# Kernel optimization log

Hardware: AMD Instinct MI355X
Metric: run time of the kernel (lower is better)

## Reference

```python
import jax, jax.numpy as jnp
import numpy as np

D_MODEL = 1024
IDX_DIM = 64
SEQ = 4096
D_STATE = 64
EXPAND = 1
HEADDIM = 32
D_CONV = 4
D_INNER = EXPAND * D_MODEL
NHEADS = D_INNER // HEADDIM
CONV_DIM = D_INNER + 2 * D_STATE
D_IN_PROJ = 2 * D_INNER + 2 * D_STATE + NHEADS  # z, xBC, dt


def setup_inputs() -> dict:
    key = jax.random.key(0)
    ks = jax.random.split(key, 8)
    def rn(k, shape, scale=1.0):
        return jax.random.normal(k, shape, jnp.float32) * scale
    return {
        "x": rn(ks[0], (SEQ, D_MODEL)),
        "W_in": rn(ks[1], (D_IN_PROJ, D_MODEL), D_MODEL ** -0.5),
        "conv_w": rn(ks[2], (CONV_DIM, D_CONV), D_CONV ** -0.5),
        "conv_b": jnp.zeros((CONV_DIM,), jnp.float32),
        "dt_bias": rn(ks[3], (NHEADS,)),
        "A_log": jnp.log(jnp.arange(1, NHEADS + 1, dtype=jnp.float32)),
        "D": jnp.ones((NHEADS,), jnp.float32),
        "norm_w": jnp.ones((D_INNER,), jnp.float32),
        "W_out": rn(ks[4], (D_MODEL, D_INNER), D_INNER ** -0.5),
        "W_q": rn(ks[5], (IDX_DIM, D_MODEL), D_MODEL ** -0.5),
        "W_k": rn(ks[6], (IDX_DIM, D_MODEL), D_MODEL ** -0.5),
    }


def _silu(v):
    return v * jax.nn.sigmoid(v)


def _mamba2(x, W_in, conv_w, conv_b, dt_bias, A_log, Dp, norm_w, W_out):
    L = x.shape[0]
    zxbcdt = x @ W_in.T  # [L, D_IN_PROJ]
    z, xBC, dt = jnp.split(zxbcdt, [D_INNER, D_INNER + CONV_DIM], axis=-1)
    # depthwise causal conv1d, kernel D_CONV
    xc = jax.lax.conv_general_dilated(
        xBC.T[None],               # [1, C, L]
        conv_w[:, None, :],        # [C, 1, K]
        (1,), [(D_CONV - 1, 0)], feature_group_count=CONV_DIM)[0].T
    xBC = _silu(xc + conv_b)
    xs, B, C = jnp.split(xBC, [D_INNER, D_INNER + D_STATE], axis=-1)
    xs = xs.reshape(L, NHEADS, HEADDIM)
    dt = jax.nn.softplus(dt + dt_bias)   # [L, H]
    A = -jnp.exp(A_log)                  # [H]

    def step(h, inp):
        x_t, B_t, C_t, dt_t = inp        # [H,P], [N], [N], [H]
        dA = jnp.exp(dt_t * A)           # [H]
        h = h * dA[:, None, None] + (dt_t[:, None] * x_t)[:, :, None] * B_t[None, None, :]
        return h, jnp.einsum('hpn,n->hp', h, C_t)

    h0 = jnp.zeros((NHEADS, HEADDIM, D_STATE), x.dtype)
    _, ys = jax.lax.scan(step, h0, (xs, B, C, dt))  # ys: [L, H, P]
    y = ys + Dp[None, :, None] * xs
    y = y.reshape(L, D_INNER)
    y = y * _silu(z)                                 # gated RMSNorm
    y = y * jax.lax.rsqrt(jnp.mean(y * y, axis=-1, keepdims=True) + 1e-5) * norm_w
    return y @ W_out.T


def reference(x, W_in, conv_w, conv_b, dt_bias, A_log, D, norm_w, W_out, W_q, W_k):
    L = x.shape[0]
    x_mamba = _mamba2(x, W_in, conv_w, conv_b, dt_bias, A_log, D, norm_w, W_out)
    q = x_mamba @ W_q.T                  # [L, IDX_DIM]
    k = x @ W_k.T                        # [L, IDX_DIM]
    scores = jnp.einsum('ti,si->ts', q, k) * (IDX_DIM ** -0.5)
    mask = jnp.tril(jnp.ones((L, L), dtype=bool))
    return jnp.where(mask, scores, -jnp.inf)
```

## Files before the change

kernel.cpp:

```cpp
#include <hip/hip_runtime.h>
#include <math.h>

#define L_SEQ 4096
#define DMODEL 1024
#define DINNER 1024
#define DSTATE 64
#define NH 32
#define HD 32
#define CONVD 1152
#define DPROJ2 2272
#define KOFF 2208
#define QC 128
#define NC 32

#define NEG_FILL (-1e30f)

typedef __attribute__((ext_vector_type(8))) short short8;
typedef __attribute__((ext_vector_type(4))) float f32x4;
typedef unsigned short u16;

__device__ __forceinline__ u16 f2bf(float f) {
  unsigned int u = __float_as_uint(f);
  unsigned int r = (u + 0x7fffu + ((u >> 16) & 1u)) >> 16;
  return (u16)r;
}
__device__ __forceinline__ float bf2f(u16 b) {
  unsigned int u = ((unsigned int)b) << 16;
  return __uint_as_float(u);
}
__device__ __forceinline__ short8 pack8(float4 a, float4 b) {
  short8 v;
  v[0] = (short)f2bf(a.x); v[1] = (short)f2bf(a.y);
  v[2] = (short)f2bf(a.z); v[3] = (short)f2bf(a.w);
  v[4] = (short)f2bf(b.x); v[5] = (short)f2bf(b.y);
  v[6] = (short)f2bf(b.z); v[7] = (short)f2bf(b.w);
  return v;
}

__device__ __forceinline__ void g2l16(const void* g, void* l) {
  __builtin_amdgcn_global_load_lds(
      (const __attribute__((address_space(1))) unsigned int*)g,
      (__attribute__((address_space(3))) unsigned int*)l, 16, 0, 0);
}

#define CAST_N0 (L_SEQ * DMODEL / 8)
#define CAST_N1 (2208 * DMODEL / 8)
#define CAST_N2 (64 * DMODEL / 8)
#define CAST_TOTAL (CAST_N0 + CAST_N1 + 2 * CAST_N2)
#define CAST_BLKS (CAST_TOTAL / 256)
__global__ __launch_bounds__(256) void cast_tr_k(const float* __restrict__ x,
                                                 const float* __restrict__ W_in,
                                                 const float* __restrict__ W_k,
                                                 const float* __restrict__ W_q,
                                                 const float* __restrict__ W_out,
                                                 u16* __restrict__ x_bf,
                                                 u16* __restrict__ Wcat,
                                                 u16* __restrict__ Wq_bf,
                                                 u16* __restrict__ WoutT) {
  __shared__ float tile[64][65];
  int bid = blockIdx.x;
  if (bid < CAST_BLKS) {
    int gid = bid * 256 + threadIdx.x;
    const float* src;
    u16* dst;
    int i;
    if (gid < CAST_N0) { src = x; dst = x_bf; i = gid; }
    else if (gid < CAST_N0 + CAST_N1) { src = W_in; dst = Wcat; i = gid - CAST_N0; }
    else if (gid < CAST_N0 + CAST_N1 + CAST_N2) {
      src = W_k; dst = Wcat + (size_t)2208 * DMODEL; i = gid - CAST_N0 - CAST_N1;
    } else { src = W_q; dst = Wq_bf; i = gid - CAST_N0 - CAST_N1 - CAST_N2; }
    i *= 8;
    float4 f0 = *(const float4*)(src + i);
    float4 f1 = *(const float4*)(src + i + 4);
    *(short8*)(dst + i) = pack8(f0, f1);
    return;
  }
  bid -= CAST_BLKS;
  int bx = bid & 15, by = bid >> 4;
  int tx = threadIdx.x & 63, ty = threadIdx.x >> 6;
#pragma unroll
  for (int k = 0; k < 16; k++) {
    int r = ty + k * 4;
    tile[r][tx] = W_out[(size_t)(by * 64 + r) * 1024 + bx * 64 + tx];
  }
  __syncthreads();
#pragma unroll
  for (int k = 0; k < 16; k++) {
    int r = ty + k * 4;
    WoutT[(size_t)(bx * 64 + r) * 1024 + by * 64 + tx] = f2bf(tile[tx][r]);
  }
}

__global__ __launch_bounds__(256) void wqo_k(const u16* __restrict__ Wq,
                                             const u16* __restrict__ WoutT,
                                             const float* __restrict__ nw,
                                             u16* __restrict__ Wqo) {
  const int tid = threadIdx.x;
  const int wave = tid >> 6, lane = tid & 63;
  const int l15 = lane & 15, quad = lane >> 4;
  const int j0 = blockIdx.x * 64;
  f32x4 acc[4] = {};
  for (int kk = 0; kk < 32; kk++) {
    short8 b = *(const short8*)(WoutT + (size_t)(j0 + wave * 16 + l15) * 1024 + kk * 32 + quad * 8);
#pragma unroll
    for (int mi = 0; mi < 4; mi++) {
      short8 a = *(const short8*)(Wq + (size_t)(mi * 16 + l15) * 1024 + kk * 32 + quad * 8);
      acc[mi] = __builtin_amdgcn_mfma_f32_16x16x32_bf16(a, b, acc[mi], 0, 0, 0);
    }
  }
  int col = j0 + wave * 16 + l15;
  float w = nw[col];
#pragma unroll
  for (int mi = 0; mi < 4; mi++)
#pragma unroll
    for (int r = 0; r < 4; r++) {
      int i = mi * 16 + quad * 4 + r;
      Wqo[(size_t)i * 1024 + col] = f2bf(acc[mi][r] * w);
    }
}

__global__ __launch_bounds__(256) void gemm128(const u16* __restrict__ A,
                                               const u16* __restrict__ B,
                                               u16* __restrict__ Cbf,
                                               int M, int N, int K) {
  __shared__ u16 As[128 * 64];
  __shared__ u16 Bs[128 * 64];
  const int tid = threadIdx.x;
  const int wave = tid >> 6, lane = tid & 63;
  const int m0 = blockIdx.x * 128, n0 = blockIdx.y * 128;
  const int wm = (wave >> 1) * 64, wn = (wave & 1) * 64;
  const int l15 = lane & 15, quad = lane >> 4;

  const u16* aptr[4];
  const u16* bptr[4];
  char *ldsA[4], *ldsB[4];
#pragma unroll
  for (int b = 0; b < 4; b++) {
    int ch = b * 256 + tid;
    int row = ch >> 3, q = (ch & 7) ^ (row & 7);
    aptr[b] = A + (size_t)(m0 + row) * K + q * 8;
    int bn = min(n0 + row, N - 1);
    bptr[b] = B + (size_t)bn * K + q * 8;
    ldsA[b] = (char*)As + b * 4096 + wave * 1024;
    ldsB[b] = (char*)Bs + b * 4096 + wave * 1024;
  }

  int offA[2][4], offB[2][4];
#pragma unroll
  for (int kk = 0; kk < 2; kk++)
#pragma unroll
    for (int i = 0; i < 4; i++) {
      int ra = wm + i * 16 + l15;
      offA[kk][i] = ra * 64 + ((kk * 4 + quad) ^ (ra & 7)) * 8;
      int rb = wn + i * 16 + l15;
      offB[kk][i] = rb * 64 + ((kk * 4 + quad) ^ (rb & 7)) * 8;
    }

  f32x4 acc[4][4] = {};
  for (int k0 = 0; k0 < K; k0 += 64) {
#pragma unroll
    for (int b = 0; b < 4; b++) g2l16(aptr[b] + k0, ldsA[b]);
#pragma unroll
    for (int b = 0; b < 4; b++) g2l16(bptr[b] + k0, ldsB[b]);
    __builtin_amdgcn_s_waitcnt(0);
    __syncthreads();
#pragma unroll
    for (int kk = 0; kk < 2; kk++) {
      short8 af[4], bfr[4];
#pragma unroll
      for (int i = 0; i < 4; i++) af[i] = *(const short8*)(As + offA[kk][i]);
#pragma unroll
      for (int j = 0; j < 4; j++) bfr[j] = *(const short8*)(Bs + offB[kk][j]);
#pragma unroll
      for (int mi = 0; mi < 4; mi++)
#pragma unroll
        for (int ni = 0; ni < 4; ni++)
          acc[mi][ni] = __builtin_amdgcn_mfma_f32_16x16x32_bf16(af[mi], bfr[ni],
                                                                acc[mi][ni], 0, 0, 0);
    }
    __syncthreads();
  }
#pragma unroll
  for (int mi = 0; mi < 4; mi++)
#pragma unroll
    for (int r = 0; r < 4; r++) {
      int grow = m0 + wm + mi * 16 + quad * 4 + r;
#pragma unroll
      for (int ni = 0; ni < 4; ni++) {
        int gcol = n0 + wn + ni * 16 + l15;
        if (gcol < N) Cbf[(size_t)grow * N + gcol] = f2bf(acc[mi][ni][r]);
      }
    }
}

__global__ __launch_bounds__(256) void splitk64(const u16* __restrict__ A,
                                                const u16* __restrict__ B,
                                                float* __restrict__ P,
                                                int M, int K) {
  __shared__ u16 As[128 * 32];
  __shared__ u16 Bs[64 * 32];
  const int tid = threadIdx.x;
  const int wave = tid >> 6, lane = tid & 63;
  const int m0 = blockIdx.x * 128;
  const int ks = blockIdx.y;
  const int wm = (wave >> 1) * 64, wn = (wave & 1) * 32;
  const int l15 = lane & 15, quad = lane >> 4;

  const int c0 = tid, c1 = 256 + tid;
  const int r0 = c0 >> 2, q0 = (c0 & 3) ^ ((r0 >> 1) & 3);
  const int r1 = c1 >> 2, q1 = (c1 & 3) ^ ((r1 >> 1) & 3);
  const int rb = tid >> 2, qb = (tid & 3) ^ ((rb >> 1) & 3);
  const u16* a0 = A + (size_t)(m0 + r0) * K + q0 * 8;
  const u16* a1 = A + (size_t)(m0 + r1) * K + q1 * 8;
  const u16* bptr = B + (size_t)rb * K + qb * 8;
  char* ldsA0 = (char*)As + wave * 1024;
  char* ldsA1 = (char*)As + 4096 + wave * 1024;
  char* ldsB = (char*)Bs + wave * 1024;

  int offA[4], offB[2];
#pragma unroll
  for (int i = 0; i < 4; i++) {
    int ra = wm + i * 16 + l15;
    offA[i] = ra * 32 + (quad ^ ((ra >> 1) & 3)) * 8;
  }
#pragma unroll
  for (int j = 0; j < 2; j++) {
    int rr = wn + j * 16 + l15;
    offB[j] = rr * 32 + (quad ^ ((rr >> 1) & 3)) * 8;
  }

  f32x4 acc[4][2] = {};
  const int kbeg = ks * 128;
  for (int k0 = kbeg; k0 < kbeg + 128; k0 += 32) {
    g2l16(a0 + k0, ldsA0);
    g2l16(a1 + k0, ldsA1);
    g2l16(bptr + k0, ldsB);
    __builtin_amdgcn_s_waitcnt(0);
    __syncthreads();
    short8 af[4], bfr[2];
#pragma unroll
    for (int i = 0; i < 4; i++) af[i] = *(const short8*)(As + offA[i]);
#pragma unroll
    for (int j = 0; j < 2; j++) bfr[j] = *(const short8*)(Bs + offB[j]);
#pragma unroll
    for (int mi = 0; mi < 4; mi++)
#pragma unroll
      for (int ni = 0; ni < 2; ni++)
        acc[mi][ni] = __builtin_amdgcn_mfma_f32_16x16x32_bf16(af[mi], bfr[ni],
                                                              acc[mi][ni], 0, 0, 0);
    __syncthreads();
  }
  float* Pp = P + (size_t)ks * M * 64;
#pragma unroll
  for (int mi = 0; mi < 4; mi++)
#pragma unroll
    for (int r = 0; r < 4; r++) {
      int grow = m0 + wm + mi * 16 + quad * 4 + r;
#pragma unroll
      for (int ni = 0; ni < 2; ni++)
        Pp[(size_t)grow * 64 + wn + ni * 16 + l15] = acc[mi][ni][r];
    }
}

__global__ __launch_bounds__(256) void reduce8_k(const float* __restrict__ P,
                                                 const float* __restrict__ ssq,
                                                 u16* __restrict__ out, int n) {
  int i = blockIdx.x * 256 + threadIdx.x;
  if (i >= n) return;
  float s = 0.f;
#pragma unroll
  for (int ks = 0; ks < 8; ks++) s += P[(size_t)ks * n + i];
  float sc = rsqrtf(ssq[i >> 6] * (1.f / 1024.f) + 1e-5f);
  out[i] = f2bf(s * sc);
}

#define CONV_BLKS (L_SEQ * 144 / 256)
__global__ __launch_bounds__(256) void conv_dt_k(const u16* __restrict__ zx,
                                                 const float* __restrict__ cw,
                                                 const float* __restrict__ cb,
                                                 u16* __restrict__ xbc,
                                                 const float* __restrict__ dt_bias,
                                                 const float* __restrict__ A_log,
                                                 float* __restrict__ dtsp,
                                                 float* __restrict__ aL,
                                                 float* __restrict__ ssq) {
  if (blockIdx.x < CONV_BLKS) {
    int gid = blockIdx.x * 256 + threadIdx.x;
    int t = gid / 144;
    int c0 = (gid - t * 144) * 8;
    float acc[8];
#pragma unroll
    for (int j = 0; j < 8; j++) acc[j] = cb[c0 + j];
    float wv[8][4];
#pragma unroll
    for (int j = 0; j < 8; j++) {
      float4 w4 = *(const float4*)(cw + (c0 + j) * 4);
      wv[j][0] = w4.x; wv[j][1] = w4.y; wv[j][2] = w4.z; wv[j][3] = w4.w;
    }
#pragma unroll
    for (int k = 0; k < 4; k++) {
      int s = t - 3 + k;
      if (s >= 0) {
        short8 v = *(const short8*)(zx + (size_t)s * DPROJ2 + DINNER + c0);
#pragma unroll
        for (int j = 0; j < 8; j++) acc[j] += bf2f((u16)v[j]) * wv[j][k];
      }
    }
    short8 o;
#pragma unroll
    for (int j = 0; j < 8; j++) o[j] = (short)f2bf(acc[j] / (1.f + expf(-acc[j])));
    *(short8*)(xbc + (size_t)t * CONVD + c0) = o;
    return;
  }
  if (threadIdx.x < 16) ssq[(blockIdx.x - CONV_BLKS) * 16 + threadIdx.x] = 0.f;
  int w = threadIdx.x >> 6, lane = threadIdx.x & 63;
  int idx = (blockIdx.x - CONV_BLKS) * 4 + w;
  int h = idx & 31, c = idx >> 5;
  float negA = -expf(A_log[h]);
  float bias = dt_bias[h];
  float carry = 0.f;
#pragma unroll
  for (int seg = 0; seg < 2; seg++) {
    int t = c * QC + seg * 64 + lane;
    float xv = bf2f(zx[(size_t)t * DPROJ2 + 2176 + h]) + bias;
    float sp = (xv > 20.f) ? xv : log1pf(expf(xv));
    dtsp[(size_t)t * 32 + h] = sp;
    float v = sp * negA;
#pragma unroll
    for (int off = 1; off < 64; off <<= 1) {
      float u = __shfl_up(v, off, 64);
      if (lane >= off) v += u;
    }
    aL[(size_t)t * 32 + h] = carry + v;
    carry += __shfl(v, 63, 64);
  }
}

__global__ __launch_bounds__(256) void csg_k(const u16* __restrict__ xbc,
                                             const float* __restrict__ dtsp,
                                             const float* __restrict__ aL,
                                             float* __restrict__ S,
                                             float* __restrict__ G) {
  int tid = threadIdx.x;
  const int wave = tid >> 6, lane = tid & 63;
  const int l15 = lane & 15, quad = lane >> 4;
  __shared__ __align__(16) u16 sXs[32 * 136];
  __shared__ __align__(16) u16 sBT[64 * 136];
  __shared__ float scoef[QC];
  if (blockIdx.x < (unsigned)(NC * NH)) {
    int h = blockIdx.x & 31, c = blockIdx.x >> 5;
    if (tid < QC) {
      float aend = aL[(size_t)(c * QC + QC - 1) * 32 + h];
      float a = aL[(size_t)(c * QC + tid) * 32 + h];
      scoef[tid] = expf(aend - a) * dtsp[(size_t)(c * QC + tid) * 32 + h];
    }
    __syncthreads();
    for (int j = tid; j < 32 * QC / 8; j += 256) {
      int s = j & 127, p0 = (j >> 7) * 8;
      short8 v = *(const short8*)(xbc + (size_t)(c * QC + s) * CONVD + h * HD + p0);
      float cf = scoef[s];
#pragma unroll
      for (int e = 0; e < 8; e++) sXs[(p0 + e) * 136 + s] = f2bf(cf * bf2f((u16)v[e]));
    }
    for (int j = tid; j < 64 * QC / 8; j += 256) {
      int s = j & 127, n0 = (j >> 7) * 8;
      short8 v = *(const short8*)(xbc + (size_t)(c * QC + s) * CONVD + DINNER + n0);
#pragma unroll
      for (int e = 0; e < 8; e++) sBT[(n0 + e) * 136 + s] = (u16)v[e];
    }
    __syncthreads();
    f32x4 acc[2] = {};
#pragma unroll
    for (int kk = 0; kk < 4; kk++) {
      short8 b = *(const short8*)(sBT + (wave * 16 + l15) * 136 + kk * 32 + quad * 8);
#pragma unroll
      for (int i = 0; i < 2; i++) {
        short8 a = *(const short8*)(sXs + (i * 16 + l15) * 136 + kk * 32 + quad * 8);
        acc[i] = __builtin_amdgcn_mfma_f32_16x16x32_bf16(a, b, acc[i], 0, 0, 0);
      }
    }
    float* Sb = S + ((size_t)c * 32 + h) * 2048;
#pragma unroll
    for (int i = 0; i < 2; i++)
#pragma unroll
      for (int r = 0; r < 4; r++) {
        int p = i * 16 + quad * 4 + r;
        Sb[p * 64 + wave * 16 + l15] = acc[i][r];
      }
    return;
  }
  int c = blockIdx.x - NC * NH;
  const int wm = (wave >> 1) * 64, wn = (wave & 1) * 64;
  f32x4 acc[4][4] = {};
#pragma unroll
  for (int kk = 0; kk < 2; kk++) {
    short8 a[4], b[4];
#pragma unroll
    for (int i = 0; i < 4; i++) {
      int t = wm + i * 16 + l15;
      a[i] = *(const short8*)(xbc + (size_t)(c * QC + t) * CONVD + DINNER + DSTATE + kk * 32 + quad * 8);
      int s = wn + i * 16 + l15;
      b[i] = *(const short8*)(xbc + (size_t)(c * QC + s) * CONVD + DINNER + kk * 32 + quad * 8);
    }
#pragma unroll
    for (int mi = 0; mi < 4; mi++)
#pragma unroll
      for (int ni = 0; ni < 4; ni++)
        acc[mi][ni] = __builtin_amdgcn_mfma_f32_16x16x32_bf16(a[mi], b[ni],
                                                              acc[mi][ni], 0, 0, 0);
  }
  float* Gb = G + (size_t)c * QC * QC;
#pragma unroll
  for (int mi = 0; mi < 4; mi++)
#pragma unroll
    for (int r = 0; r < 4; r++) {
      int t = wm + mi * 16 + quad * 4 + r;
#pragma unroll
      for (int ni = 0; ni < 4; ni++)
        Gb[(size_t)t * QC + wn + ni * 16 + l15] = acc[mi][ni][r];
    }
}

__global__ __launch_bounds__(256) void state_scan_k(const float* __restrict__ S,
                                                    const float* __restrict__ aL,
                                                    float* __restrict__ Hinit) {
  int idx = blockIdx.x * 256 + threadIdx.x;
  int h = idx >> 11, rem = idx & 2047;
  float E = 0.f;
#pragma unroll
  for (int c = 0; c < NC; c++) {
    size_t o = ((size_t)c * 32 + h) * 2048 + rem;
    Hinit[o] = E;
    float dec = expf(aL[(size_t)(c * QC + QC - 1) * 32 + h]);
    E = E * dec + S[o];
  }
}

__global__ __launch_bounds__(256) void yout_mfma(const u16* __restrict__ xbc,
                                                 const float* __restrict__ dtsp,
                                                 const float* __restrict__ aL,
                                                 const float* __restrict__ G,
                                                 const float* __restrict__ Hinit,
                                                 const float* __restrict__ Dv,
                                                 const u16* __restrict__ zx,
                                                 float* __restrict__ ssq,
                                                 u16* __restrict__ y) {
  int h = blockIdx.x & 31, c = blockIdx.x >> 5;
  int tid = threadIdx.x;
  __shared__ __align__(16) u16 sXT[32 * 136];
  __shared__ float sa[QC];
  __shared__ float sd[QC];

  if (tid < QC) {
    sa[tid] = aL[(size_t)(c * QC + tid) * 32 + h];
    sd[tid] = dtsp[(size_t)(c * QC + tid) * 32 + h];
  }
  for (int j = tid; j < 32 * QC / 8; j += 256) {
    int t = j & 127, p0 = (j >> 7) * 8;
    short8 v = *(const short8*)(xbc + (size_t)(c * QC + t) * CONVD + h * HD + p0);
#pragma unroll
    for (int e = 0; e < 8; e++) sXT[(p0 + e) * 136 + t] = (u16)v[e];
  }
  __syncthreads();

  const int wave = tid >> 6, lane = tid & 63;
  const int l15 = lane & 15, quad = lane >> 4;
  f32x4 acc1[2][2] = {};
  f32x4 acc2[2][2] = {};

#pragma unroll
  for (int kk = 0; kk < 4; kk++) {
    short8 b[2];
#pragma unroll
    for (int j = 0; j < 2; j++)
      b[j] = *(const short8*)(sXT + (j * 16 + l15) * 136 + kk * 32 + quad * 8);
#pragma unroll
    for (int i = 0; i < 2; i++) {
      int rmax = wave * 32 + i * 16 + 15;
      if (kk * 32 > rmax) continue;
      int m = wave * 32 + i * 16 + l15;
      float am = sa[m];
      const float* Gp = G + (size_t)c * QC * QC + (size_t)m * QC + kk * 32 + quad * 8;
      float4 g0 = *(const float4*)Gp;
      float4 g1 = *(const float4*)(Gp + 4);
      float gv[8] = {g0.x, g0.y, g0.z, g0.w, g1.x, g1.y, g1.z, g1.w};
      int s0 = kk * 32 + quad * 8;
      short8 a;
#pragma unroll
      for (int j2 = 0; j2 < 8; j2++) {
        int s = s0 + j2;
        float w = 0.f;
        if (s <= m) w = expf(am - sa[s]) * sd[s] * gv[j2];
        a[j2] = (short)f2bf(w);
      }
#pragma unroll
      for (int j = 0; j < 2; j++)
        acc1[i][j] = __builtin_amdgcn_mfma_f32_16x16x32_bf16(a, b[j], acc1[i][j], 0, 0, 0);
    }
  }

  const float* Hbase = Hinit + ((size_t)c * 32 + h) * 2048;
#pragma unroll
  for (int kk = 0; kk < 2; kk++) {
    short8 b[2];
#pragma unroll
    for (int j = 0; j < 2; j++) {
      const float* Hp = Hbase + (size_t)(j * 16 + l15) * 64 + kk * 32 + quad * 8;
      b[j] = pack8(*(const float4*)Hp, *(const float4*)(Hp + 4));
    }
#pragma unroll
    for (int i = 0; i < 2; i++) {
      int t = wave * 32 + i * 16 + l15;
      short8 a = *(const short8*)(xbc + (size_t)(c * QC + t) * CONVD + DINNER + DSTATE + kk * 32 + quad * 8);
#pragma unroll
      for (int j = 0; j < 2; j++)
        acc2[i][j] = __builtin_amdgcn_mfma_f32_16x16x32_bf16(a, b[j], acc2[i][j], 0, 0, 0);
    }
  }

  float Dh = Dv[h];
#pragma unroll
  for (int i = 0; i < 2; i++) {
#pragma unroll
    for (int r = 0; r < 4; r++) {
      int t = wave * 32 + i * 16 + quad * 4 + r;
      float et = expf(sa[t]);
      float part = 0.f;
#pragma unroll
      for (int j = 0; j < 2; j++) {
        int p = j * 16 + l15;
        float xv = bf2f(sXT[p * 136 + t]);
        float val = acc1[i][j][r] + et * acc2[i][j][r] + Dh * xv;
        float z = bf2f(zx[(size_t)(c * QC + t) * DPROJ2 + h * HD + p]);
        float vg = val * (z / (1.f + expf(-z)));
        part += vg * vg;
        y[(size_t)(c * QC + t) * DINNER + h * HD + p] = f2bf(vg);
      }
      part += __shfl_xor(part, 1, 64);
      part += __shfl_xor(part, 2, 64);
      part += __shfl_xor(part, 4, 64);
      part += __shfl_xor(part, 8, 64);
      if (l15 == 0) atomicAdd(ssq + c * QC + t, part);
    }
  }
}

__global__ __launch_bounds__(256) void scores_mfma(const u16* __restrict__ q,
                                                   const u16* __restrict__ kmat,
                                                   int kstride,
                                                   float* __restrict__ out) {
  const int m0 = blockIdx.y * 128, n0 = blockIdx.x * 128;
  const int tid = threadIdx.x;
  if (n0 > m0 + 127) {
    f32x4 f = {NEG_FILL, NEG_FILL, NEG_FILL, NEG_FILL};
    for (int i = tid; i < 128 * 32; i += 256) {
      int row = i >> 5, c4 = (i & 31) << 2;
      __builtin_nontemporal_store(f, (f32x4*)(out + (size_t)(m0 + row) * L_SEQ + n0 + c4));
    }
    return;
  }
  const int wave = tid >> 6, lane = tid & 63;
  const int wm = (wave >> 1) * 64, wn = (wave & 1) * 64;
  const int l15 = lane & 15, quad = lane >> 4;
  f32x4 acc[4][4] = {};
#pragma unroll
  for (int kk = 0; kk < 2; kk++) {
    short8 a[4], b[4];
#pragma unroll
    for (int i = 0; i < 4; i++) {
      a[i] = *(const short8*)(q + (size_t)(m0 + wm + i * 16 + l15) * 64 + kk * 32 + quad * 8);
      b[i] = *(const short8*)(kmat + (size_t)(n0 + wn + i * 16 + l15) * kstride + kk * 32 + quad * 8);
    }
#pragma unroll
    for (int mi = 0; mi < 4; mi++)
#pragma unroll
      for (int ni = 0; ni < 4; ni++)
        acc[mi][ni] = __builtin_amdgcn_mfma_f32_16x16x32_bf16(a[mi], b[ni],
                                                              acc[mi][ni], 0, 0, 0);
  }
#pragma unroll
  for (int mi = 0; mi < 4; mi++)
#pragma unroll
    for (int r = 0; r < 4; r++) {
      int row = m0 + wm + mi * 16 + quad * 4 + r;
#pragma unroll
      for (int ni = 0; ni < 4; ni++) {
        int col = n0 + wn + ni * 16 + l15;
        float val = (col <= row) ? acc[mi][ni][r] * 0.125f : NEG_FILL;
        __builtin_nontemporal_store(val, out + (size_t)row * L_SEQ + col);
      }
    }
}

extern "C" void kernel_launch(void* const* d_in, const int* in_sizes, int n_in,
                              void* d_out, int out_size, void* d_ws, size_t ws_size,
                              hipStream_t stream) {
  const float* x       = (const float*)d_in[0];
  const float* W_in    = (const float*)d_in[1];
  const float* conv_w  = (const float*)d_in[2];
  const float* conv_b  = (const float*)d_in[3];
  const float* dt_bias = (const float*)d_in[4];
  const float* A_log   = (const float*)d_in[5];
  const float* Dv      = (const float*)d_in[6];
  const float* norm_w  = (const float*)d_in[7];
  const float* W_out   = (const float*)d_in[8];
  const float* W_q     = (const float*)d_in[9];
  const float* W_k     = (const float*)d_in[10];
  float* out = (float*)d_out;

  char* ws = (char*)d_ws;
  size_t off = 0;
  auto alloc = [&](size_t bytes) {
    void* p = (void*)(ws + off);
    off += (bytes + 255) & ~(size_t)255;
    return p;
  };
  u16* zx_bf    = (u16*)alloc((size_t)L_SEQ * DPROJ2 * 2);
  u16* xbc_bf   = (u16*)alloc((size_t)L_SEQ * CONVD * 2);
  float* dtsp   = (float*)alloc((size_t)L_SEQ * NH * 4);
  float* aL     = (float*)alloc((size_t)L_SEQ * NH * 4);
  float* S      = (float*)alloc((size_t)NC * NH * HD * DSTATE * 4);
  float* Hinit  = (float*)alloc((size_t)NC * NH * HD * DSTATE * 4);
  float* G      = (float*)alloc((size_t)NC * QC * QC * 4);
  float* ssq    = (float*)alloc((size_t)L_SEQ * 4);
  u16* y1_bf    = (u16*)alloc((size_t)L_SEQ * DINNER * 2);
  u16* x_bf     = (u16*)alloc((size_t)L_SEQ * DMODEL * 2);
  u16* Wcat_bf  = (u16*)alloc((size_t)DPROJ2 * DMODEL * 2);
  u16* WoutT_bf = (u16*)alloc((size_t)DMODEL * DINNER * 2);
  u16* Wq_bf    = (u16*)alloc((size_t)64 * DMODEL * 2);
  u16* Wqo_bf   = (u16*)alloc((size_t)64 * DINNER * 2);
  u16* q_bf     = (u16*)alloc((size_t)L_SEQ * 64 * 2);
  float* Pq = S;

  cast_tr_k<<<dim3(CAST_BLKS + 256), 256, 0, stream>>>(x, W_in, W_k, W_q, W_out,
                                                       x_bf, Wcat_bf, Wq_bf, WoutT_bf);
  wqo_k<<<dim3(16), 256, 0, stream>>>(Wq_bf, WoutT_bf, norm_w, Wqo_bf);
  gemm128<<<dim3(L_SEQ / 128, (DPROJ2 + 127) / 128), 256, 0, stream>>>(
      x_bf, Wcat_bf, zx_bf, L_SEQ, DPROJ2, DMODEL);
  conv_dt_k<<<dim3(CONV_BLKS + NC * NH / 4), 256, 0, stream>>>(
      zx_bf, conv_w, conv_b, xbc_bf, dt_bias, A_log, dtsp, aL, ssq);
  csg_k<<<dim3(NC * NH + NC), 256, 0, stream>>>(xbc_bf, dtsp, aL, S, G);
  state_scan_k<<<dim3(NH * HD * DSTATE / 256), 256, 0, stream>>>(S, aL, Hinit);
  yout_mfma<<<dim3(NC * NH), 256, 0, stream>>>(xbc_bf, dtsp, aL, G, Hinit, Dv,
                                               zx_bf, ssq, y1_bf);
  splitk64<<<dim3(L_SEQ / 128, 8), 256, 0, stream>>>(y1_bf, Wqo_bf, Pq, L_SEQ, DINNER);
  reduce8_k<<<dim3(L_SEQ * 64 / 256), 256, 0, stream>>>(Pq, ssq, q_bf, L_SEQ * 64);
  scores_mfma<<<dim3(32, 32), 256, 0, stream>>>(q_bf, zx_bf + KOFF, DPROJ2, out);
}
```

Before: 240.4 us.

## Fuse small kernels, move masked fill earlier, replace split-K q GEMM

Merges the Wq·Wout precompute into the input-projection GEMM launch and replaces the split-K q GEMM plus reduce with a single full-K GEMM that applies the RMS scale and the 1/8 factor in its epilogue. It also copies the k columns into a compact buffer inside the conv kernel, moves the upper-triangle -inf fill into the csg kernel so it overlaps other work, and stores Hinit in bf16. Together these cut launch count, partial-sum traffic and strided reads, at the cost of less parallelism in the q GEMM and extra bf16 rounding of Hinit.

New measurement: 223.5 us. 1.08x faster.

```diff
diff --git a/kernel.cpp b/kernel.cpp
--- a/kernel.cpp
+++ b/kernel.cpp
@@ -91,45 +91,45 @@
   }
 }
 
-__global__ __launch_bounds__(256) void wqo_k(const u16* __restrict__ Wq,
-                                             const u16* __restrict__ WoutT,
-                                             const float* __restrict__ nw,
-                                             u16* __restrict__ Wqo) {
-  const int tid = threadIdx.x;
-  const int wave = tid >> 6, lane = tid & 63;
-  const int l15 = lane & 15, quad = lane >> 4;
-  const int j0 = blockIdx.x * 64;
-  f32x4 acc[4] = {};
-  for (int kk = 0; kk < 32; kk++) {
-    short8 b = *(const short8*)(WoutT + (size_t)(j0 + wave * 16 + l15) * 1024 + kk * 32 + quad * 8);
-#pragma unroll
-    for (int mi = 0; mi < 4; mi++) {
-      short8 a = *(const short8*)(Wq + (size_t)(mi * 16 + l15) * 1024 + kk * 32 + quad * 8);
-      acc[mi] = __builtin_amdgcn_mfma_f32_16x16x32_bf16(a, b, acc[mi], 0, 0, 0);
-    }
-  }
-  int col = j0 + wave * 16 + l15;
-  float w = nw[col];
-#pragma unroll
-  for (int mi = 0; mi < 4; mi++)
-#pragma unroll
-    for (int r = 0; r < 4; r++) {
-      int i = mi * 16 + quad * 4 + r;
-      Wqo[(size_t)i * 1024 + col] = f2bf(acc[mi][r] * w);
-    }
-}
-
-__global__ __launch_bounds__(256) void gemm128(const u16* __restrict__ A,
-                                               const u16* __restrict__ B,
-                                               u16* __restrict__ Cbf,
-                                               int M, int N, int K) {
+#define GEMM_BLKS 576
+__global__ __launch_bounds__(256) void gemm_wqo_k(const u16* __restrict__ A,
+                                                  const u16* __restrict__ B,
+                                                  u16* __restrict__ Cbf,
+                                                  const u16* __restrict__ Wq,
+                                                  const u16* __restrict__ WoutT,
+                                                  const float* __restrict__ nw,
+                                                  u16* __restrict__ Wqo) {
   __shared__ u16 As[128 * 64];
   __shared__ u16 Bs[128 * 64];
   const int tid = threadIdx.x;
   const int wave = tid >> 6, lane = tid & 63;
-  const int m0 = blockIdx.x * 128, n0 = blockIdx.y * 128;
+  const int l15 = lane & 15, quad = lane >> 4;
+  const int wg = blockIdx.x;
+  if (wg >= GEMM_BLKS) {
+    const int j0 = (wg - GEMM_BLKS) * 64;
+    f32x4 acc[4] = {};
+    for (int kk = 0; kk < 32; kk++) {
+      short8 b = *(const short8*)(WoutT + (size_t)(j0 + wave * 16 + l15) * 1024 + kk * 32 + quad * 8);
+#pragma unroll
+      for (int mi = 0; mi < 4; mi++) {
+        short8 a = *(const short8*)(Wq + (size_t)(mi * 16 + l15) * 1024 + kk * 32 + quad * 8);
+        acc[mi] = __builtin_amdgcn_mfma_f32_16x16x32_bf16(a, b, acc[mi], 0, 0, 0);
+      }
+    }
+    int col = j0 + wave * 16 + l15;
+    float w = nw[col];
+#pragma unroll
+    for (int mi = 0; mi < 4; mi++)
+#pragma unroll
+      for (int r = 0; r < 4; r++) {
+        int i = mi * 16 + quad * 4 + r;
+        Wqo[(size_t)i * 1024 + col] = f2bf(acc[mi][r] * w);
+      }
+    return;
+  }
+  const int M = L_SEQ, N = DPROJ2, K = DMODEL;
+  const int m0 = (wg & 31) * 128, n0 = (wg >> 5) * 128;
   const int wm = (wave >> 1) * 64, wn = (wave & 1) * 64;
-  const int l15 = lane & 15, quad = lane >> 4;
 
   const u16* aptr[4];
   const u16* bptr[4];
@@ -193,101 +193,87 @@
     }
 }
 
-__global__ __launch_bounds__(256) void splitk64(const u16* __restrict__ A,
-                                                const u16* __restrict__ B,
-                                                float* __restrict__ P,
-                                                int M, int K) {
-  __shared__ u16 As[128 * 32];
-  __shared__ u16 Bs[64 * 32];
+__global__ __launch_bounds__(256) void qgemm_k(const u16* __restrict__ A,
+                                               const u16* __restrict__ B,
+                                               const float* __restrict__ ssq,
+                                               u16* __restrict__ q) {
+  __shared__ u16 As[32 * 64];
+  __shared__ u16 Bs[64 * 64];
   const int tid = threadIdx.x;
   const int wave = tid >> 6, lane = tid & 63;
-  const int m0 = blockIdx.x * 128;
-  const int ks = blockIdx.y;
-  const int wm = (wave >> 1) * 64, wn = (wave & 1) * 32;
+  const int m0 = blockIdx.x * 32;
+  const int wm = (wave >> 1) * 16, wn = (wave & 1) * 32;
   const int l15 = lane & 15, quad = lane >> 4;
-
-  const int c0 = tid, c1 = 256 + tid;
-  const int r0 = c0 >> 2, q0 = (c0 & 3) ^ ((r0 >> 1) & 3);
-  const int r1 = c1 >> 2, q1 = (c1 & 3) ^ ((r1 >> 1) & 3);
-  const int rb = tid >> 2, qb = (tid & 3) ^ ((rb >> 1) & 3);
-  const u16* a0 = A + (size_t)(m0 + r0) * K + q0 * 8;
-  const u16* a1 = A + (size_t)(m0 + r1) * K + q1 * 8;
-  const u16* bptr = B + (size_t)rb * K + qb * 8;
-  char* ldsA0 = (char*)As + wave * 1024;
-  char* ldsA1 = (char*)As + 4096 + wave * 1024;
-  char* ldsB = (char*)Bs + wave * 1024;
-
-  int offA[4], offB[2];
-#pragma unroll
-  for (int i = 0; i < 4; i++) {
-    int ra = wm + i * 16 + l15;
-    offA[i] = ra * 32 + (quad ^ ((ra >> 1) & 3)) * 8;
-  }
-#pragma unroll
-  for (int j = 0; j < 2; j++) {
-    int rr = wn + j * 16 + l15;
-    offB[j] = rr * 32 + (quad ^ ((rr >> 1) & 3)) * 8;
-  }
-
-  f32x4 acc[4][2] = {};
-  const int kbeg = ks * 128;
-  for (int k0 = kbeg; k0 < kbeg + 128; k0 += 32) {
-    g2l16(a0 + k0, ldsA0);
-    g2l16(a1 + k0, ldsA1);
-    g2l16(bptr + k0, ldsB);
+  const int K = 1024;
+
+  int rowA = tid >> 3, qA = (tid & 7) ^ (rowA & 7);
+  const u16* aptr = A + (size_t)(m0 + rowA) * K + qA * 8;
+  char* ldsA = (char*)As + wave * 1024;
+  const u16* bptr[2];
+  char* ldsB[2];
+#pragma unroll
+  for (int b = 0; b < 2; b++) {
+    int ch = b * 256 + tid;
+    int row = ch >> 3, qq = (ch & 7) ^ (row & 7);
+    bptr[b] = B + (size_t)row * K + qq * 8;
+    ldsB[b] = (char*)Bs + b * 4096 + wave * 1024;
+  }
+  int offA[2], offB[2][2];
+#pragma unroll
+  for (int kk = 0; kk < 2; kk++) {
+    int ra = wm + l15;
+    offA[kk] = ra * 64 + ((kk * 4 + quad) ^ (ra & 7)) * 8;
+#pragma unroll
+    for (int j = 0; j < 2; j++) {
+      int rb = wn + j * 16 + l15;
+      offB[kk][j] = rb * 64 + ((kk * 4 + quad) ^ (rb & 7)) * 8;
+    }
+  }
+  f32x4 acc[2] = {};
+  for (int k0 = 0; k0 < K; k0 += 64) {
+    g2l16(aptr + k0, ldsA);
+#pragma unroll
+    for (int b = 0; b < 2; b++) g2l16(bptr[b] + k0, ldsB[b]);
     __builtin_amdgcn_s_waitcnt(0);
     __syncthreads();
-    short8 af[4], bfr[2];
-#pragma unroll
-    for (int i = 0; i < 4; i++) af[i] = *(const short8*)(As + offA[i]);
-#pragma unroll
-    for (int j = 0; j < 2; j++) bfr[j] = *(const short8*)(Bs + offB[j]);
-#pragma unroll
-    for (int mi = 0; mi < 4; mi++)
-#pragma unroll
-      for (int ni = 0; ni < 2; ni++)
-        acc[mi][ni] = __builtin_amdgcn_mfma_f32_16x16x32_bf16(af[mi], bfr[ni],
-                                                              acc[mi][ni], 0, 0, 0);
+#pragma unroll
+    for (int kk = 0; kk < 2; kk++) {
+      short8 af = *(const short8*)(As + offA[kk]);
+#pragma unroll
+      for (int j = 0; j < 2; j++) {
+        short8 bf8 = *(const short8*)(Bs + offB[kk][j]);
+        acc[j] = __builtin_amdgcn_mfma_f32_16x16x32_bf16(af, bf8, acc[j], 0, 0, 0);
+      }
+    }
     __syncthreads();
   }
-  float* Pp = P + (size_t)ks * M * 64;
-#pragma unroll
-  for (int mi = 0; mi < 4; mi++)
-#pragma unroll
-    for (int r = 0; r < 4; r++) {
-      int grow = m0 + wm + mi * 16 + quad * 4 + r;
-#pragma unroll
-      for (int ni = 0; ni < 2; ni++)
-        Pp[(size_t)grow * 64 + wn + ni * 16 + l15] = acc[mi][ni][r];
-    }
-}
-
-__global__ __launch_bounds__(256) void reduce8_k(const float* __restrict__ P,
-                                                 const float* __restrict__ ssq,
-                                                 u16* __restrict__ out, int n) {
-  int i = blockIdx.x * 256 + threadIdx.x;
-  if (i >= n) return;
-  float s = 0.f;
-#pragma unroll
-  for (int ks = 0; ks < 8; ks++) s += P[(size_t)ks * n + i];
-  float sc = rsqrtf(ssq[i >> 6] * (1.f / 1024.f) + 1e-5f);
-  out[i] = f2bf(s * sc);
-}
-
-#define CONV_BLKS (L_SEQ * 144 / 256)
+#pragma unroll
+  for (int r = 0; r < 4; r++) {
+    int grow = m0 + wm + quad * 4 + r;
+    float sc = rsqrtf(ssq[grow] * (1.f / 1024.f) + 1e-5f) * 0.125f;
+#pragma unroll
+    for (int j = 0; j < 2; j++)
+      q[(size_t)grow * 64 + wn + j * 16 + l15] = f2bf(acc[j][r] * sc);
+  }
+}
+
+#define CONVB 2304
+#define KDB 128
 __global__ __launch_bounds__(256) void conv_dt_k(const u16* __restrict__ zx,
                                                  const float* __restrict__ cw,
                                                  const float* __restrict__ cb,
                                                  u16* __restrict__ xbc,
+                                                 u16* __restrict__ kd,
                                                  const float* __restrict__ dt_bias,
                                                  const float* __restrict__ A_log,
                                                  float* __restrict__ dtsp,
                                                  float* __restrict__ aL,
                                                  float* __restrict__ ssq) {
-  if (blockIdx.x < CONV_BLKS) {
-    int gid = blockIdx.x * 256 + threadIdx.x;
-    int t = gid / 144;
-    int c0 = (gid - t * 144) * 8;
+  int bid = blockIdx.x, tid = threadIdx.x;
+  if (bid < CONVB) {
+    int tblk = bid / 9, cgb = bid - tblk * 9;
+    int t = tblk * 16 + (tid >> 4);
+    int c0 = (cgb * 16 + (tid & 15)) * 8;
     float acc[8];
 #pragma unroll
     for (int j = 0; j < 8; j++) acc[j] = cb[c0 + j];
@@ -312,9 +298,17 @@
     *(short8*)(xbc + (size_t)t * CONVD + c0) = o;
     return;
   }
-  if (threadIdx.x < 16) ssq[(blockIdx.x - CONV_BLKS) * 16 + threadIdx.x] = 0.f;
-  int w = threadIdx.x >> 6, lane = threadIdx.x & 63;
-  int idx = (blockIdx.x - CONV_BLKS) * 4 + w;
+  if (bid < CONVB + KDB) {
+    int gid = (bid - CONVB) * 256 + tid;
+    int t = gid >> 3, c0 = (gid & 7) * 8;
+    *(short8*)(kd + (size_t)t * 64 + c0) =
+        *(const short8*)(zx + (size_t)t * DPROJ2 + KOFF + c0);
+    return;
+  }
+  int dblk = bid - CONVB - KDB;
+  if (tid < 16) ssq[dblk * 16 + tid] = 0.f;
+  int w = tid >> 6, lane = tid & 63;
+  int idx = dblk * 4 + w;
   int h = idx & 31, c = idx >> 5;
   float negA = -expf(A_log[h]);
   float bias = dt_bias[h];
@@ -340,7 +334,8 @@
                                              const float* __restrict__ dtsp,
                                              const float* __restrict__ aL,
                                              float* __restrict__ S,
-                                             float* __restrict__ G) {
+                                             float* __restrict__ G,
+                                             float* __restrict__ out) {
   int tid = threadIdx.x;
   const int wave = tid >> 6, lane = tid & 63;
   const int l15 = lane & 15, quad = lane >> 4;
@@ -389,48 +384,62 @@
       }
     return;
   }
-  int c = blockIdx.x - NC * NH;
-  const int wm = (wave >> 1) * 64, wn = (wave & 1) * 64;
-  f32x4 acc[4][4] = {};
-#pragma unroll
-  for (int kk = 0; kk < 2; kk++) {
-    short8 a[4], b[4];
-#pragma unroll
-    for (int i = 0; i < 4; i++) {
-      int t = wm + i * 16 + l15;
-      a[i] = *(const short8*)(xbc + (size_t)(c * QC + t) * CONVD + DINNER + DSTATE + kk * 32 + quad * 8);
-      int s = wn + i * 16 + l15;
-      b[i] = *(const short8*)(xbc + (size_t)(c * QC + s) * CONVD + DINNER + kk * 32 + quad * 8);
-    }
+  if (blockIdx.x < (unsigned)(NC * NH + NC)) {
+    int c = blockIdx.x - NC * NH;
+    const int wm = (wave >> 1) * 64, wn = (wave & 1) * 64;
+    f32x4 acc[4][4] = {};
+#pragma unroll
+    for (int kk = 0; kk < 2; kk++) {
+      short8 a[4], b[4];
+#pragma unroll
+      for (int i = 0; i < 4; i++) {
+        int t = wm + i * 16 + l15;
+        a[i] = *(const short8*)(xbc + (size_t)(c * QC + t) * CONVD + DINNER + DSTATE + kk * 32 + quad * 8);
+        int s = wn + i * 16 + l15;
+        b[i] = *(const short8*)(xbc + (size_t)(c * QC + s) * CONVD + DINNER + kk * 32 + quad * 8);
+      }
+#pragma unroll
+      for (int mi = 0; mi < 4; mi++)
+#pragma unroll
+        for (int ni = 0; ni < 4; ni++)
+          acc[mi][ni] = __builtin_amdgcn_mfma_f32_16x16x32_bf16(a[mi], b[ni],
+                                                                acc[mi][ni], 0, 0, 0);
+    }
+    float* Gb = G + (size_t)c * QC * QC;
 #pragma unroll
     for (int mi = 0; mi < 4; mi++)
 #pragma unroll
-      for (int ni = 0; ni < 4; ni++)
-        acc[mi][ni] = __builtin_amdgcn_mfma_f32_16x16x32_bf16(a[mi], b[ni],
-                                                              acc[mi][ni], 0, 0, 0);
-  }
-  float* Gb = G + (size_t)c * QC * QC;
-#pragma unroll
-  for (int mi = 0; mi < 4; mi++)
-#pragma unroll
-    for (int r = 0; r < 4; r++) {
-      int t = wm + mi * 16 + quad * 4 + r;
-#pragma unroll
-      for (int ni = 0; ni < 4; ni++)
-        Gb[(size_t)t * QC + wn + ni * 16 + l15] = acc[mi][ni][r];
-    }
+      for (int r = 0; r < 4; r++) {
+        int t = wm + mi * 16 + quad * 4 + r;
+#pragma unroll
+        for (int ni = 0; ni < 4; ni++)
+          Gb[(size_t)t * QC + wn + ni * 16 + l15] = acc[mi][ni][r];
+      }
+    return;
+  }
+  int f = blockIdx.x - (NC * NH + NC);
+  int u = f / 31, v = f - u * 31;
+  int by, bx;
+  if (v >= u) { by = u; bx = v + 1; }
+  else { by = 31 - u; bx = 32 - u + v; }
+  int m0 = by * 128, n0 = bx * 128;
+  f32x4 fl = {NEG_FILL, NEG_FILL, NEG_FILL, NEG_FILL};
+  for (int i = tid; i < 128 * 32; i += 256) {
+    int row = i >> 5, c4 = (i & 31) << 2;
+    __builtin_nontemporal_store(fl, (f32x4*)(out + (size_t)(m0 + row) * L_SEQ + n0 + c4));
+  }
 }
 
 __global__ __launch_bounds__(256) void state_scan_k(const float* __restrict__ S,
                                                     const float* __restrict__ aL,
-                                                    float* __restrict__ Hinit) {
+                                                    u16* __restrict__ Hinit) {
   int idx = blockIdx.x * 256 + threadIdx.x;
   int h = idx >> 11, rem = idx & 2047;
   float E = 0.f;
 #pragma unroll
   for (int c = 0; c < NC; c++) {
     size_t o = ((size_t)c * 32 + h) * 2048 + rem;
-    Hinit[o] = E;
+    Hinit[o] = f2bf(E);
     float dec = expf(aL[(size_t)(c * QC + QC - 1) * 32 + h]);
     E = E * dec + S[o];
   }
@@ -440,7 +449,7 @@
                                                  const float* __restrict__ dtsp,
                                                  const float* __restrict__ aL,
                                                  const float* __restrict__ G,
-                                                 const float* __restrict__ Hinit,
+                                                 const u16* __restrict__ Hinit,
                                                  const float* __restrict__ Dv,
                                                  const u16* __restrict__ zx,
                                                  float* __restrict__ ssq,
@@ -499,15 +508,13 @@
     }
   }
 
-  const float* Hbase = Hinit + ((size_t)c * 32 + h) * 2048;
+  const u16* Hbase = Hinit + ((size_t)c * 32 + h) * 2048;
 #pragma unroll
   for (int kk = 0; kk < 2; kk++) {
     short8 b[2];
 #pragma unroll
-    for (int j = 0; j < 2; j++) {
-      const float* Hp = Hbase + (size_t)(j * 16 + l15) * 64 + kk * 32 + quad * 8;
-      b[j] = pack8(*(const float4*)Hp, *(const float4*)(Hp + 4));
-    }
+    for (int j = 0; j < 2; j++)
+      b[j] = *(const short8*)(Hbase + (size_t)(j * 16 + l15) * 64 + kk * 32 + quad * 8);
 #pragma unroll
     for (int i = 0; i < 2; i++) {
       int t = wave * 32 + i * 16 + l15;
@@ -546,19 +553,11 @@
 }
 
 __global__ __launch_bounds__(256) void scores_mfma(const u16* __restrict__ q,
-                                                   const u16* __restrict__ kmat,
-                                                   int kstride,
+                                                   const u16* __restrict__ kd,
                                                    float* __restrict__ out) {
   const int m0 = blockIdx.y * 128, n0 = blockIdx.x * 128;
+  if (n0 > m0 + 127) return;
   const int tid = threadIdx.x;
-  if (n0 > m0 + 127) {
-    f32x4 f = {NEG_FILL, NEG_FILL, NEG_FILL, NEG_FILL};
-    for (int i = tid; i < 128 * 32; i += 256) {
-      int row = i >> 5, c4 = (i & 31) << 2;
-      __builtin_nontemporal_store(f, (f32x4*)(out + (size_t)(m0 + row) * L_SEQ + n0 + c4));
-    }
-    return;
-  }
   const int wave = tid >> 6, lane = tid & 63;
   const int wm = (wave >> 1) * 64, wn = (wave & 1) * 64;
   const int l15 = lane & 15, quad = lane >> 4;
@@ -569,7 +568,7 @@
 #pragma unroll
     for (int i = 0; i < 4; i++) {
       a[i] = *(const short8*)(q + (size_t)(m0 + wm + i * 16 + l15) * 64 + kk * 32 + quad * 8);
-      b[i] = *(const short8*)(kmat + (size_t)(n0 + wn + i * 16 + l15) * kstride + kk * 32 + quad * 8);
+      b[i] = *(const short8*)(kd + (size_t)(n0 + wn + i * 16 + l15) * 64 + kk * 32 + quad * 8);
     }
 #pragma unroll
     for (int mi = 0; mi < 4; mi++)
@@ -586,7 +585,7 @@
 #pragma unroll
       for (int ni = 0; ni < 4; ni++) {
         int col = n0 + wn + ni * 16 + l15;
-        float val = (col <= row) ? acc[mi][ni][r] * 0.125f : NEG_FILL;
+        float val = (col <= row) ? acc[mi][ni][r] : NEG_FILL;
         __builtin_nontemporal_store(val, out + (size_t)row * L_SEQ + col);
       }
     }
@@ -620,30 +619,28 @@
   float* dtsp   = (float*)alloc((size_t)L_SEQ * NH * 4);
   float* aL     = (float*)alloc((size_t)L_SEQ * NH * 4);
   float* S      = (float*)alloc((size_t)NC * NH * HD * DSTATE * 4);
-  float* Hinit  = (float*)alloc((size_t)NC * NH * HD * DSTATE * 4);
+  u16* Hinit    = (u16*)alloc((size_t)NC * NH * HD * DSTATE * 2);
   float* G      = (float*)alloc((size_t)NC * QC * QC * 4);
   float* ssq    = (float*)alloc((size_t)L_SEQ * 4);
   u16* y1_bf    = (u16*)alloc((size_t)L_SEQ * DINNER * 2);
+  u16* kd_bf    = (u16*)alloc((size_t)L_SEQ * 64 * 2);
   u16* x_bf     = (u16*)alloc((size_t)L_SEQ * DMODEL * 2);
   u16* Wcat_bf  = (u16*)alloc((size_t)DPROJ2 * DMODEL * 2);
   u16* WoutT_bf = (u16*)alloc((size_t)DMODEL * DINNER * 2);
   u16* Wq_bf    = (u16*)alloc((size_t)64 * DMODEL * 2);
   u16* Wqo_bf   = (u16*)alloc((size_t)64 * DINNER * 2);
   u16* q_bf     = (u16*)alloc((size_t)L_SEQ * 64 * 2);
-  float* Pq = S;
 
   cast_tr_k<<<dim3(CAST_BLKS + 256), 256, 0, stream>>>(x, W_in, W_k, W_q, W_out,
                                                        x_bf, Wcat_bf, Wq_bf, WoutT_bf);
-  wqo_k<<<dim3(16), 256, 0, stream>>>(Wq_bf, WoutT_bf, norm_w, Wqo_bf);
-  gemm128<<<dim3(L_SEQ / 128, (DPROJ2 + 127) / 128), 256, 0, stream>>>(
-      x_bf, Wcat_bf, zx_bf, L_SEQ, DPROJ2, DMODEL);
-  conv_dt_k<<<dim3(CONV_BLKS + NC * NH / 4), 256, 0, stream>>>(
-      zx_bf, conv_w, conv_b, xbc_bf, dt_bias, A_log, dtsp, aL, ssq);
-  csg_k<<<dim3(NC * NH + NC), 256, 0, stream>>>(xbc_bf, dtsp, aL, S, G);
+  gemm_wqo_k<<<dim3(GEMM_BLKS + 16), 256, 0, stream>>>(x_bf, Wcat_bf, zx_bf,
+                                                       Wq_bf, WoutT_bf, norm_w, Wqo_bf);
+  conv_dt_k<<<dim3(CONVB + KDB + 256), 256, 0, stream>>>(
+      zx_bf, conv_w, conv_b, xbc_bf, kd_bf, dt_bias, A_log, dtsp, aL, ssq);
+  csg_k<<<dim3(NC * NH + NC + 496), 256, 0, stream>>>(xbc_bf, dtsp, aL, S, G, out);
   state_scan_k<<<dim3(NH * HD * DSTATE / 256), 256, 0, stream>>>(S, aL, Hinit);
   yout_mfma<<<dim3(NC * NH), 256, 0, stream>>>(xbc_bf, dtsp, aL, G, Hinit, Dv,
                                                zx_bf, ssq, y1_bf);
-  splitk64<<<dim3(L_SEQ / 128, 8), 256, 0, stream>>>(y1_bf, Wqo_bf, Pq, L_SEQ, DINNER);
-  reduce8_k<<<dim3(L_SEQ * 64 / 256), 256, 0, stream>>>(Pq, ssq, q_bf, L_SEQ * 64);
-  scores_mfma<<<dim3(32, 32), 256, 0, stream>>>(q_bf, zx_bf + KOFF, DPROJ2, out);
-}
+  qgemm_k<<<dim3(L_SEQ / 32), 256, 0, stream>>>(y1_bf, Wqo_bf, ssq, q_bf);
+  scores_mfma<<<dim3(32, 32), 256, 0, stream>>>(q_bf, kd_bf, out);
+}
```
